# Optimization experiments

Hardware: AMD Instinct MI355X
Metric: run time of the kernel (lower is better)

Reference implementation:

```python
import jax, jax.numpy as jnp
import numpy as np

N_PTS = 32768      # n_x == n_y (query points == source points)
K_NBR = 32         # neighbors per query point
N_EDGES = N_PTS * K_NBR
D_COORD = 3
C = 64             # f_y channels == MLP output channels
H = 256            # MLP hidden width


def setup_inputs() -> dict:
    key = jax.random.key(0)
    ks = jax.random.split(key, 12)
    y = jax.random.normal(ks[0], (N_PTS, D_COORD), dtype=jnp.float32)
    x = jax.random.normal(ks[1], (N_PTS, D_COORD), dtype=jnp.float32)
    f_y = jax.random.normal(ks[2], (N_PTS, C), dtype=jnp.float32)
    neighbors_index = jax.random.randint(ks[3], (N_EDGES,), 0, N_PTS, dtype=jnp.int64)
    neighbors_row_splits = (jnp.arange(N_PTS + 1, dtype=jnp.int64) * K_NBR)
    weights = jax.random.uniform(ks[4], (N_EDGES,), dtype=jnp.float32)
    # LinearChannelMLP params: layers [6, 256, 256, 64], gelu between layers
    def dense(k, fan_in, fan_out):
        w = jax.random.normal(k, (fan_in, fan_out), dtype=jnp.float32) / np.sqrt(fan_in)
        return w
    W0 = dense(ks[5], 2 * D_COORD, H)
    b0 = jnp.zeros((H,), dtype=jnp.float32)
    W1 = dense(ks[6], H, H)
    b1 = jnp.zeros((H,), dtype=jnp.float32)
    W2 = dense(ks[7], H, C)
    b2 = jnp.zeros((C,), dtype=jnp.float32)
    return {"y": y, "x": x, "f_y": f_y,
            "neighbors_index": neighbors_index,
            "neighbors_row_splits": neighbors_row_splits,
            "weights": weights,
            "W0": W0, "b0": b0, "W1": W1, "b1": b1, "W2": W2, "b2": b2}


def reference(y, x, f_y, neighbors_index, neighbors_row_splits, weights,
              W0, b0, W1, b1, W2, b2):
    n_x = neighbors_row_splits.shape[0] - 1
    n_edges = neighbors_index.shape[0]
    # CSR row id for each edge (equivalent to repeat(arange(n_x), num_reps))
    seg = jnp.searchsorted(neighbors_row_splits, jnp.arange(n_edges), side='right') - 1
    rep_features = y[neighbors_index]            # [E, 3] gathered source coords
    self_features = x[seg]                       # [E, 3] repeated query coords
    agg = jnp.concatenate([rep_features, self_features], axis=-1)  # [E, 6]
    # channel MLP (gelu between layers, none after last)
    h = jax.nn.gelu(agg @ W0 + b0)
    h = jax.nn.gelu(h @ W1 + b1)
    rep = h @ W2 + b2                            # [E, C] kernel values
    # transform_type='linear': kernel * f_y(neighbor)
    rep = rep * f_y[neighbors_index]
    # quadrature weights (forces sum reduction, as in source)
    rep = rep * weights[:, None]
    out = jax.ops.segment_sum(rep, seg, num_segments=n_x)  # segment-CSR sum
    return out
```

## Files before the change

kernel.cpp:

```cpp
#include <hip/hip_runtime.h>
#include <hip/hip_bf16.h>
#include <stdint.h>

#define NPTS 32768
#define KNBR 32
#define NEDGES (NPTS * KNBR)
#define TM 64
#define AGG_STRIDE 40
#define H_STRIDE 264

typedef __attribute__((ext_vector_type(8))) short short8;
typedef __attribute__((ext_vector_type(4))) float f32x4;
typedef __attribute__((ext_vector_type(4))) unsigned int u32x4;
typedef __attribute__((ext_vector_type(2))) unsigned int u32x2;

__device__ __forceinline__ unsigned short f2bf(float f) {
    unsigned int u = __float_as_uint(f);
    unsigned int r = (u + 0x7FFFu + ((u >> 16) & 1u)) >> 16;
    return (unsigned short)r;
}

__device__ __forceinline__ unsigned int pack2bf(float a, float b) {
    return (unsigned int)f2bf(a) | ((unsigned int)f2bf(b) << 16);
}

__device__ __forceinline__ void store_h4(unsigned short* p, float a, float b, float c, float d) {
    u32x2 v;
    v.x = pack2bf(a, b);
    v.y = pack2bf(c, d);
    *reinterpret_cast<u32x2*>(p) = v;
}

__device__ __forceinline__ float gelu_tanh(float x) {
    float x2 = x * x;
    float u = fmaf(-0.102942496f, x2, -2.30220824f);
    float e = __builtin_amdgcn_exp2f(x * u);
    return x * __builtin_amdgcn_rcpf(1.0f + e);
}

__global__ void pack_w(const float* __restrict__ W0, const float* __restrict__ W1,
                       const float* __restrict__ W2, unsigned short* __restrict__ wp) {
    int tid = blockIdx.x * blockDim.x + threadIdx.x;
    if (tid >= 11264) return;
    unsigned short v[8];
    int l = tid & 63;
    if (tid < 1024) {
        int nt = tid >> 6;
        int n = nt * 16 + (l & 15);
        int k0 = (l >> 4) << 3;
        #pragma unroll
        for (int j = 0; j < 8; ++j) {
            int k = k0 + j;
            v[j] = f2bf(k < 6 ? W0[k * 256 + n] : 0.0f);
        }
    } else if (tid < 9216) {
        int q = tid - 1024;
        int nt = (q >> 6) & 15;
        int s = q >> 10;
        int n = nt * 16 + (l & 15);
        int k0 = s * 32 + ((l >> 4) << 3);
        #pragma unroll
        for (int j = 0; j < 8; ++j) v[j] = f2bf(W1[(k0 + j) * 256 + n]);
    } else {
        int q = tid - 9216;
        int nt = (q >> 6) & 3;
        int s = q >> 8;
        int n = nt * 16 + (l & 15);
        int k0 = s * 32 + ((l >> 4) << 3);
        #pragma unroll
        for (int j = 0; j < 8; ++j) v[j] = f2bf(W2[(k0 + j) * 64 + n]);
    }
    unsigned short* o = &wp[tid * 8];
    #pragma unroll
    for (int j = 0; j < 8; ++j) o[j] = v[j];
}

__global__ __launch_bounds__(256, 3)
void gno_fused(const float* __restrict__ y, const float* __restrict__ x,
               const float* __restrict__ f_y, const int* __restrict__ nbr,
               const float* __restrict__ wts,
               const float* __restrict__ b0, const float* __restrict__ b1,
               const float* __restrict__ b2,
               const unsigned short* __restrict__ wp,
               float* __restrict__ out) {
    __shared__ __align__(16) unsigned short agg_lds[TM * AGG_STRIDE];
    __shared__ __align__(16) unsigned short h_lds[TM * H_STRIDE];

    const int b = blockIdx.x;
    const int tid = threadIdx.x;
    const int l = tid & 63;
    const int w = tid >> 6;
    const int lg = l >> 4;
    const int ln = l & 15;
    const int ebase = b * TM;

    if (tid < TM) {
        int e = ebase + tid;
        int j = nbr[e];
        int i = e >> 5;
        const float* yr = &y[j * 3];
        const float* xr = &x[i * 3];
        u32x4 q0;
        q0.x = pack2bf(yr[0], yr[1]);
        q0.y = pack2bf(yr[2], xr[0]);
        q0.z = pack2bf(xr[1], xr[2]);
        q0.w = 0u;
        u32x4 z = {0u, 0u, 0u, 0u};
        unsigned short* row = &agg_lds[tid * AGG_STRIDE];
        *(u32x4*)(row +  0) = q0;
        *(u32x4*)(row +  8) = z;
        *(u32x4*)(row + 16) = z;
        *(u32x4*)(row + 24) = z;
    }
    __syncthreads();

    {
        short8 aw[4];
        f32x4 b0v[4];
        #pragma unroll
        for (int n = 0; n < 4; ++n) {
            int nt = 4 * w + n;
            aw[n] = *(const short8*)&wp[(nt * 64 + l) * 8];
            b0v[n] = *(const f32x4*)&b0[nt * 16 + lg * 4];
        }
        f32x4 zero = {0.f, 0.f, 0.f, 0.f};
        #pragma unroll
        for (int mt = 0; mt < 4; ++mt) {
            short8 ag = *(const short8*)&agg_lds[(mt * 16 + ln) * AGG_STRIDE + lg * 8];
            #pragma unroll
            for (int n = 0; n < 4; ++n) {
                f32x4 c = __builtin_amdgcn_mfma_f32_16x16x32_bf16(aw[n], ag, zero, 0, 0, 0);
                float g0 = gelu_tanh(c[0] + b0v[n][0]);
                float g1 = gelu_tanh(c[1] + b0v[n][1]);
                float g2 = gelu_tanh(c[2] + b0v[n][2]);
                float g3 = gelu_tanh(c[3] + b0v[n][3]);
                store_h4(&h_lds[(mt * 16 + ln) * H_STRIDE + (4 * w + n) * 16 + lg * 4],
                         g0, g1, g2, g3);
            }
        }
    }
    __syncthreads();

    f32x4 acc[4][4];
    #pragma unroll
    for (int mt = 0; mt < 4; ++mt)
        #pragma unroll
        for (int n = 0; n < 4; ++n)
            acc[mt][n] = (f32x4){0.f, 0.f, 0.f, 0.f};

    #pragma unroll
    for (int s = 0; s < 8; ++s) {
        short8 aw[4];
        #pragma unroll
        for (int n = 0; n < 4; ++n)
            aw[n] = *(const short8*)&wp[(1024 + (s * 16 + 4 * w + n) * 64 + l) * 8];
        #pragma unroll
        for (int mt = 0; mt < 4; ++mt) {
            short8 hb = *(const short8*)&h_lds[(mt * 16 + ln) * H_STRIDE + s * 32 + lg * 8];
            #pragma unroll
            for (int n = 0; n < 4; ++n)
                acc[mt][n] = __builtin_amdgcn_mfma_f32_16x16x32_bf16(aw[n], hb, acc[mt][n], 0, 0, 0);
        }
    }
    __syncthreads();

    {
        f32x4 b1v[4];
        #pragma unroll
        for (int n = 0; n < 4; ++n) b1v[n] = *(const f32x4*)&b1[(4 * w + n) * 16 + lg * 4];
        #pragma unroll
        for (int mt = 0; mt < 4; ++mt) {
            #pragma unroll
            for (int n = 0; n < 4; ++n) {
                float g0 = gelu_tanh(acc[mt][n][0] + b1v[n][0]);
                float g1 = gelu_tanh(acc[mt][n][1] + b1v[n][1]);
                float g2 = gelu_tanh(acc[mt][n][2] + b1v[n][2]);
                float g3 = gelu_tanh(acc[mt][n][3] + b1v[n][3]);
                store_h4(&h_lds[(mt * 16 + ln) * H_STRIDE + (4 * w + n) * 16 + lg * 4],
                         g0, g1, g2, g3);
            }
        }
    }
    __syncthreads();

    f32x4 acc3[4];
    #pragma unroll
    for (int mt = 0; mt < 4; ++mt) acc3[mt] = (f32x4){0.f, 0.f, 0.f, 0.f};

    #pragma unroll
    for (int s = 0; s < 8; ++s) {
        short8 aw = *(const short8*)&wp[(9216 + (s * 4 + w) * 64 + l) * 8];
        #pragma unroll
        for (int mt = 0; mt < 4; ++mt) {
            short8 hb = *(const short8*)&h_lds[(mt * 16 + ln) * H_STRIDE + s * 32 + lg * 8];
            acc3[mt] = __builtin_amdgcn_mfma_f32_16x16x32_bf16(aw, hb, acc3[mt], 0, 0, 0);
        }
    }

    {
        f32x4 b2v = *(const f32x4*)&b2[w * 16 + lg * 4];
        f32x4 seg[2];
        seg[0] = (f32x4){0.f, 0.f, 0.f, 0.f};
        seg[1] = (f32x4){0.f, 0.f, 0.f, 0.f};
        #pragma unroll
        for (int mt = 0; mt < 4; ++mt) {
            int e = ebase + mt * 16 + ln;
            int j = nbr[e];
            f32x4 fy = *(const f32x4*)&f_y[j * 64 + w * 16 + lg * 4];
            float wt = wts[e];
            f32x4 v;
            #pragma unroll
            for (int i = 0; i < 4; ++i)
                v[i] = (acc3[mt][i] + b2v[i]) * fy[i] * wt;
            seg[mt >> 1] += v;
        }
        #pragma unroll
        for (int g = 0; g < 2; ++g) {
            f32x4 v = seg[g];
            #pragma unroll
            for (int d = 1; d <= 8; d <<= 1) {
                #pragma unroll
                for (int i = 0; i < 4; ++i)
                    v[i] += __shfl_xor(v[i], d, 64);
            }
            if (ln == 0)
                *(f32x4*)&out[(b * 2 + g) * 64 + w * 16 + lg * 4] = v;
        }
    }
}

extern "C" void kernel_launch(void* const* d_in, const int* in_sizes, int n_in,
                              void* d_out, int out_size, void* d_ws, size_t ws_size,
                              hipStream_t stream) {
    const float* y   = (const float*)d_in[0];
    const float* x   = (const float*)d_in[1];
    const float* f_y = (const float*)d_in[2];
    const int*   nbr = (const int*)d_in[3];
    const float* wts = (const float*)d_in[5];
    const float* W0  = (const float*)d_in[6];
    const float* b0  = (const float*)d_in[7];
    const float* W1  = (const float*)d_in[8];
    const float* b1  = (const float*)d_in[9];
    const float* W2  = (const float*)d_in[10];
    const float* b2  = (const float*)d_in[11];
    unsigned short* wp = (unsigned short*)d_ws;
    float* out = (float*)d_out;

    pack_w<<<dim3(44), dim3(256), 0, stream>>>(W0, W1, W2, wp);
    gno_fused<<<dim3(NEDGES / TM), dim3(256), 0, stream>>>(
        y, x, f_y, nbr, wts, b0, b1, b2, wp, out);
}
```

Measured before the change: 297.1 us.

## Split waves 2x2 over rows and columns, use hardware bf16 pack

```diff
diff --git a/kernel.cpp b/kernel.cpp
--- a/kernel.cpp
+++ b/kernel.cpp
@@ -20,14 +20,16 @@
     return (unsigned short)r;
 }
 
-__device__ __forceinline__ unsigned int pack2bf(float a, float b) {
-    return (unsigned int)f2bf(a) | ((unsigned int)f2bf(b) << 16);
+__device__ __forceinline__ unsigned int cvt_pk_bf16(float lo, float hi) {
+    unsigned int r;
+    asm("v_cvt_pk_bf16_f32 %0, %1, %2" : "=v"(r) : "v"(lo), "v"(hi));
+    return r;
 }
 
 __device__ __forceinline__ void store_h4(unsigned short* p, float a, float b, float c, float d) {
     u32x2 v;
-    v.x = pack2bf(a, b);
-    v.y = pack2bf(c, d);
+    v.x = cvt_pk_bf16(a, b);
+    v.y = cvt_pk_bf16(c, d);
     *reinterpret_cast<u32x2*>(p) = v;
 }
 
@@ -90,6 +92,8 @@
     const int tid = threadIdx.x;
     const int l = tid & 63;
     const int w = tid >> 6;
+    const int wm = w & 1;
+    const int wn = w >> 1;
     const int lg = l >> 4;
     const int ln = l & 15;
     const int ebase = b * TM;
@@ -101,9 +105,9 @@
         const float* yr = &y[j * 3];
         const float* xr = &x[i * 3];
         u32x4 q0;
-        q0.x = pack2bf(yr[0], yr[1]);
-        q0.y = pack2bf(yr[2], xr[0]);
-        q0.z = pack2bf(xr[1], xr[2]);
+        q0.x = cvt_pk_bf16(yr[0], yr[1]);
+        q0.y = cvt_pk_bf16(yr[2], xr[0]);
+        q0.z = cvt_pk_bf16(xr[1], xr[2]);
         q0.w = 0u;
         u32x4 z = {0u, 0u, 0u, 0u};
         unsigned short* row = &agg_lds[tid * AGG_STRIDE];
@@ -115,108 +119,119 @@
     __syncthreads();
 
     {
-        short8 aw[4];
-        f32x4 b0v[4];
-        #pragma unroll
-        for (int n = 0; n < 4; ++n) {
-            int nt = 4 * w + n;
-            aw[n] = *(const short8*)&wp[(nt * 64 + l) * 8];
-            b0v[n] = *(const f32x4*)&b0[nt * 16 + lg * 4];
-        }
+        short8 ag[2];
+        #pragma unroll
+        for (int m = 0; m < 2; ++m)
+            ag[m] = *(const short8*)&agg_lds[((2 * wm + m) * 16 + ln) * AGG_STRIDE + lg * 8];
         f32x4 zero = {0.f, 0.f, 0.f, 0.f};
         #pragma unroll
-        for (int mt = 0; mt < 4; ++mt) {
-            short8 ag = *(const short8*)&agg_lds[(mt * 16 + ln) * AGG_STRIDE + lg * 8];
-            #pragma unroll
-            for (int n = 0; n < 4; ++n) {
-                f32x4 c = __builtin_amdgcn_mfma_f32_16x16x32_bf16(aw[n], ag, zero, 0, 0, 0);
-                float g0 = gelu_tanh(c[0] + b0v[n][0]);
-                float g1 = gelu_tanh(c[1] + b0v[n][1]);
-                float g2 = gelu_tanh(c[2] + b0v[n][2]);
-                float g3 = gelu_tanh(c[3] + b0v[n][3]);
-                store_h4(&h_lds[(mt * 16 + ln) * H_STRIDE + (4 * w + n) * 16 + lg * 4],
+        for (int n = 0; n < 8; ++n) {
+            int nt = 8 * wn + n;
+            short8 aw = *(const short8*)&wp[(nt * 64 + l) * 8];
+            f32x4 b0v = *(const f32x4*)&b0[nt * 16 + lg * 4];
+            #pragma unroll
+            for (int m = 0; m < 2; ++m) {
+                int mt = 2 * wm + m;
+                f32x4 c = __builtin_amdgcn_mfma_f32_16x16x32_bf16(aw, ag[m], zero, 0, 0, 0);
+                float g0 = gelu_tanh(c[0] + b0v[0]);
+                float g1 = gelu_tanh(c[1] + b0v[1]);
+                float g2 = gelu_tanh(c[2] + b0v[2]);
+                float g3 = gelu_tanh(c[3] + b0v[3]);
+                store_h4(&h_lds[(mt * 16 + ln) * H_STRIDE + nt * 16 + lg * 4],
                          g0, g1, g2, g3);
             }
         }
     }
     __syncthreads();
 
-    f32x4 acc[4][4];
-    #pragma unroll
-    for (int mt = 0; mt < 4; ++mt)
-        #pragma unroll
-        for (int n = 0; n < 4; ++n)
-            acc[mt][n] = (f32x4){0.f, 0.f, 0.f, 0.f};
+    f32x4 acc[2][8];
+    #pragma unroll
+    for (int m = 0; m < 2; ++m)
+        #pragma unroll
+        for (int n = 0; n < 8; ++n)
+            acc[m][n] = (f32x4){0.f, 0.f, 0.f, 0.f};
 
     #pragma unroll
     for (int s = 0; s < 8; ++s) {
-        short8 aw[4];
-        #pragma unroll
-        for (int n = 0; n < 4; ++n)
-            aw[n] = *(const short8*)&wp[(1024 + (s * 16 + 4 * w + n) * 64 + l) * 8];
-        #pragma unroll
-        for (int mt = 0; mt < 4; ++mt) {
-            short8 hb = *(const short8*)&h_lds[(mt * 16 + ln) * H_STRIDE + s * 32 + lg * 8];
-            #pragma unroll
-            for (int n = 0; n < 4; ++n)
-                acc[mt][n] = __builtin_amdgcn_mfma_f32_16x16x32_bf16(aw[n], hb, acc[mt][n], 0, 0, 0);
+        short8 hb[2];
+        #pragma unroll
+        for (int m = 0; m < 2; ++m)
+            hb[m] = *(const short8*)&h_lds[((2 * wm + m) * 16 + ln) * H_STRIDE + s * 32 + lg * 8];
+        #pragma unroll
+        for (int n = 0; n < 8; ++n) {
+            short8 aw = *(const short8*)&wp[(1024 + (s * 16 + 8 * wn + n) * 64 + l) * 8];
+            #pragma unroll
+            for (int m = 0; m < 2; ++m)
+                acc[m][n] = __builtin_amdgcn_mfma_f32_16x16x32_bf16(aw, hb[m], acc[m][n], 0, 0, 0);
         }
     }
     __syncthreads();
 
     {
-        f32x4 b1v[4];
-        #pragma unroll
-        for (int n = 0; n < 4; ++n) b1v[n] = *(const f32x4*)&b1[(4 * w + n) * 16 + lg * 4];
-        #pragma unroll
-        for (int mt = 0; mt < 4; ++mt) {
-            #pragma unroll
-            for (int n = 0; n < 4; ++n) {
-                float g0 = gelu_tanh(acc[mt][n][0] + b1v[n][0]);
-                float g1 = gelu_tanh(acc[mt][n][1] + b1v[n][1]);
-                float g2 = gelu_tanh(acc[mt][n][2] + b1v[n][2]);
-                float g3 = gelu_tanh(acc[mt][n][3] + b1v[n][3]);
-                store_h4(&h_lds[(mt * 16 + ln) * H_STRIDE + (4 * w + n) * 16 + lg * 4],
+        #pragma unroll
+        for (int n = 0; n < 8; ++n) {
+            int nt = 8 * wn + n;
+            f32x4 b1v = *(const f32x4*)&b1[nt * 16 + lg * 4];
+            #pragma unroll
+            for (int m = 0; m < 2; ++m) {
+                int mt = 2 * wm + m;
+                float g0 = gelu_tanh(acc[m][n][0] + b1v[0]);
+                float g1 = gelu_tanh(acc[m][n][1] + b1v[1]);
+                float g2 = gelu_tanh(acc[m][n][2] + b1v[2]);
+                float g3 = gelu_tanh(acc[m][n][3] + b1v[3]);
+                store_h4(&h_lds[(mt * 16 + ln) * H_STRIDE + nt * 16 + lg * 4],
                          g0, g1, g2, g3);
             }
         }
     }
     __syncthreads();
 
-    f32x4 acc3[4];
-    #pragma unroll
-    for (int mt = 0; mt < 4; ++mt) acc3[mt] = (f32x4){0.f, 0.f, 0.f, 0.f};
+    f32x4 acc3[2][2];
+    #pragma unroll
+    for (int m = 0; m < 2; ++m)
+        #pragma unroll
+        for (int jj = 0; jj < 2; ++jj)
+            acc3[m][jj] = (f32x4){0.f, 0.f, 0.f, 0.f};
 
     #pragma unroll
     for (int s = 0; s < 8; ++s) {
-        short8 aw = *(const short8*)&wp[(9216 + (s * 4 + w) * 64 + l) * 8];
-        #pragma unroll
-        for (int mt = 0; mt < 4; ++mt) {
-            short8 hb = *(const short8*)&h_lds[(mt * 16 + ln) * H_STRIDE + s * 32 + lg * 8];
-            acc3[mt] = __builtin_amdgcn_mfma_f32_16x16x32_bf16(aw, hb, acc3[mt], 0, 0, 0);
+        short8 hb[2];
+        #pragma unroll
+        for (int m = 0; m < 2; ++m)
+            hb[m] = *(const short8*)&h_lds[((2 * wm + m) * 16 + ln) * H_STRIDE + s * 32 + lg * 8];
+        #pragma unroll
+        for (int jj = 0; jj < 2; ++jj) {
+            short8 aw = *(const short8*)&wp[(9216 + (s * 4 + 2 * wn + jj) * 64 + l) * 8];
+            #pragma unroll
+            for (int m = 0; m < 2; ++m)
+                acc3[m][jj] = __builtin_amdgcn_mfma_f32_16x16x32_bf16(aw, hb[m], acc3[m][jj], 0, 0, 0);
         }
     }
 
     {
-        f32x4 b2v = *(const f32x4*)&b2[w * 16 + lg * 4];
         f32x4 seg[2];
         seg[0] = (f32x4){0.f, 0.f, 0.f, 0.f};
         seg[1] = (f32x4){0.f, 0.f, 0.f, 0.f};
         #pragma unroll
-        for (int mt = 0; mt < 4; ++mt) {
-            int e = ebase + mt * 16 + ln;
+        for (int m = 0; m < 2; ++m) {
+            int e = ebase + (2 * wm + m) * 16 + ln;
             int j = nbr[e];
-            f32x4 fy = *(const f32x4*)&f_y[j * 64 + w * 16 + lg * 4];
             float wt = wts[e];
-            f32x4 v;
-            #pragma unroll
-            for (int i = 0; i < 4; ++i)
-                v[i] = (acc3[mt][i] + b2v[i]) * fy[i] * wt;
-            seg[mt >> 1] += v;
-        }
-        #pragma unroll
-        for (int g = 0; g < 2; ++g) {
-            f32x4 v = seg[g];
+            #pragma unroll
+            for (int jj = 0; jj < 2; ++jj) {
+                int ch = (2 * wn + jj) * 16 + lg * 4;
+                f32x4 fy = *(const f32x4*)&f_y[j * 64 + ch];
+                f32x4 b2v = *(const f32x4*)&b2[ch];
+                f32x4 v;
+                #pragma unroll
+                for (int i = 0; i < 4; ++i)
+                    v[i] = (acc3[m][jj][i] + b2v[i]) * fy[i] * wt;
+                seg[jj] += v;
+            }
+        }
+        #pragma unroll
+        for (int jj = 0; jj < 2; ++jj) {
+            f32x4 v = seg[jj];
             #pragma unroll
             for (int d = 1; d <= 8; d <<= 1) {
                 #pragma unroll
@@ -224,7 +239,7 @@
                     v[i] += __shfl_xor(v[i], d, 64);
             }
             if (ln == 0)
-                *(f32x4*)&out[(b * 2 + g) * 64 + w * 16 + lg * 4] = v;
+                *(f32x4*)&out[(2 * b + wm) * 64 + (2 * wn + jj) * 16 + lg * 4] = v;
         }
     }
 }
```

After: 293.9 us. No clear change (-1.1%).
